# Performance work log

Hardware: AMD Instinct MI355X
Metric: run time of the kernel (lower is better)

Reference implementation:

```python
import jax, jax.numpy as jnp
import numpy as np

OT_REG = 0.1
OT_ITERS = 10
LN_EPS = 1e-5


def layernorm(x, g, b):
    m = jnp.mean(x, axis=-1, keepdims=True)
    v = jnp.mean((x - m) ** 2, axis=-1, keepdims=True)
    return (x - m) * jax.lax.rsqrt(v + LN_EPS) * g + b


def sinkhorn(C, epsilon, iters):
    # standard Sinkhorn: kernel exp(C/eps), alternate row/col normalization
    Q = jnp.exp(C / epsilon)  # [Na,B,La,Lb]
    def body(_, Q):
        Q = Q / jnp.sum(Q, axis=-1, keepdims=True)
        Q = Q / jnp.sum(Q, axis=-2, keepdims=True)
        return Q
    return jax.lax.fori_loop(0, iters, body, Q)


def setup_inputs() -> dict:
    key = jax.random.key(0)
    ks = jax.random.split(key, 16)
    Na, La, B, Lb, Din, H = 32, 32, 64, 32, 768, 768
    s = 0.02
    return {
        "entity_cls": jax.random.normal(ks[0], (Na, Din), jnp.float32),
        "entity_tokens": jax.random.normal(ks[1], (Na, La, Din), jnp.float32),
        "mention_cls": jax.random.normal(ks[2], (B, Din), jnp.float32),
        "mention_tokens": jax.random.normal(ks[3], (B, Lb, Din), jnp.float32),
        "Wq": jax.random.normal(ks[4], (Din, H), jnp.float32) * s,
        "bq": jnp.zeros((H,), jnp.float32),
        "Wk": jax.random.normal(ks[5], (Din, H), jnp.float32) * s,
        "bk": jnp.zeros((H,), jnp.float32),
        "Wv": jax.random.normal(ks[6], (Din, H), jnp.float32) * s,
        "bv": jnp.zeros((H,), jnp.float32),
        "ln1_g": jnp.ones((H,), jnp.float32),
        "ln1_b": jnp.zeros((H,), jnp.float32),
        "Wcls": jax.random.normal(ks[7], (Din, H), jnp.float32) * s,
        "bcls": jnp.zeros((H,), jnp.float32),
        "Wsp": jax.random.normal(ks[8], (H, 1), jnp.float32) * s,
        "bsp": jnp.zeros((1,), jnp.float32),
        "ln2_g": jnp.ones((H,), jnp.float32),
        "ln2_b": jnp.zeros((H,), jnp.float32),
    }


def reference(entity_cls, entity_tokens, mention_cls, mention_tokens,
              Wq, bq, Wk, bk, Wv, bv, ln1_g, ln1_b,
              Wcls, bcls, Wsp, bsp, ln2_g, ln2_b):
    # projections
    q = entity_tokens @ Wq + bq      # [Na,La,H]
    k = mention_tokens @ Wk + bk     # [B,Lb,H]
    v = mention_tokens @ Wv + bv     # [B,Lb,H]

    # cross-batch cosine similarity: [Na,B,La,Lb]
    qn = q / jnp.maximum(jnp.linalg.norm(q, axis=-1, keepdims=True), 1e-8)
    kn = k / jnp.maximum(jnp.linalg.norm(k, axis=-1, keepdims=True), 1e-8)
    C = jnp.einsum('aid,bjd->abij', qn, kn)

    # Sinkhorn on detached cost (torch uses C.detach())
    T = sinkhorn(jax.lax.stop_gradient(C), OT_REG, OT_ITERS)
    # F.normalize(dim=-1): L2 normalize last dim
    T = T / jnp.maximum(jnp.linalg.norm(T, axis=-1, keepdims=True), 1e-12)

    # attention + residual + layernorm: [Na,B,La,H]
    attended = jnp.einsum('abij,bjd->abid', T, v) + q[:, None, :, :]
    attended = layernorm(attended, ln1_g, ln1_b)

    # softpool over token dim (-2)
    w = jax.nn.softmax(attended @ Wsp + bsp, axis=-2)   # [Na,B,La,1]
    pooled = jnp.sum(attended * w, axis=-2)             # [Na,B,H]
    context = layernorm(pooled, ln2_g, ln2_b)

    # matching scores
    ecls = entity_cls @ Wcls + bcls                     # [Na,H]
    g2l = jnp.sum(ecls[:, None, :] * context, axis=-1)  # [Na,B]
    g2l = g2l.T                                         # [B,Na]
    g2g = mention_cls @ entity_cls.T                    # [B,Na]
    return (g2l + g2g) * 0.5
```

## Files before the change

### kernel.cpp

```cpp
#include <hip/hip_runtime.h>
#include <math.h>


typedef __attribute__((ext_vector_type(8))) short bfrag8;
typedef __attribute__((ext_vector_type(4))) float f32x4;

__device__ __forceinline__ unsigned short f2bf(float x) {
  union { float f; unsigned u; } v; v.f = x;
  unsigned r = v.u + 0x7fffu + ((v.u >> 16) & 1u);
  return (unsigned short)(r >> 16);
}

__global__ __launch_bounds__(256) void prep_kernel(
    const float* __restrict__ a0, const float* __restrict__ a1, const float* __restrict__ a2,
    unsigned short* __restrict__ o0, unsigned short* __restrict__ o1, unsigned short* __restrict__ o2,
    float* __restrict__ nrm,
    const float* __restrict__ W0, const float* __restrict__ W1,
    const float* __restrict__ W2, const float* __restrict__ W3,
    unsigned short* __restrict__ T0, unsigned short* __restrict__ T1,
    unsigned short* __restrict__ T2, unsigned short* __restrict__ T3) {
  __shared__ float t[32][33];
  int bx = blockIdx.x;
  if (bx < 2331) {
    if (bx < 2328) {
      const float* in; unsigned short* out; int i, n4;
      if (bx < 768)       { in = a0; out = o0; i = bx * 256 + threadIdx.x;          n4 = 196608; }
      else if (bx < 2304) { in = a1; out = o1; i = (bx - 768) * 256 + threadIdx.x;  n4 = 393216; }
      else                { in = a2; out = o2; i = (bx - 2304) * 256 + threadIdx.x; n4 = 6144; }
      if (i >= n4) return;
      float4 f = ((const float4*)in)[i];
      ushort4 o;
      o.x = f2bf(f.x); o.y = f2bf(f.y); o.z = f2bf(f.z); o.w = f2bf(f.w);
      ((ushort4*)out)[i] = o;
    } else {
      int i = (bx - 2328) * 256 + threadIdx.x;
      if (i < 768) ((float4*)nrm)[i] = make_float4(0.f, 0.f, 0.f, 0.f);
    }
    return;
  }
  int idx = bx - 2331;
  int z = idx / 576, r2 = idx % 576;
  int tby = r2 / 24, tbx = r2 % 24;
  const float* W = (z == 0) ? W0 : (z == 1) ? W1 : (z == 2) ? W2 : W3;
  unsigned short* O = (z == 0) ? T0 : (z == 1) ? T1 : (z == 2) ? T2 : T3;
  const int gx = tbx * 32, gy = tby * 32;
  const int tx = threadIdx.x & 31, ty = threadIdx.x >> 5;
#pragma unroll
  for (int u = 0; u < 4; ++u) {
    int row = ty + u * 8;
    t[row][tx] = W[(size_t)(gy + row) * 768 + gx + tx];
  }
  __syncthreads();
#pragma unroll
  for (int u = 0; u < 4; ++u) {
    int row = ty + u * 8;
    O[(size_t)(gx + row) * 768 + gy + tx] = f2bf(t[tx][row]);
  }
}

__global__ __launch_bounds__(256) void proj_gemm_kernel(
    const unsigned short* __restrict__ Ae, const unsigned short* __restrict__ Am,
    const unsigned short* __restrict__ Acls,
    const unsigned short* __restrict__ WqT, const unsigned short* __restrict__ WkT,
    const unsigned short* __restrict__ WvT, const unsigned short* __restrict__ WclsT,
    const float* __restrict__ bq, const float* __restrict__ bk,
    const float* __restrict__ bv, const float* __restrict__ bcls,
    unsigned short* __restrict__ qb, unsigned short* __restrict__ qT,
    unsigned short* __restrict__ kb, unsigned short* __restrict__ vT,
    float* __restrict__ ecls, float* __restrict__ iq_sq, float* __restrict__ ik_sq) {
  const int z = blockIdx.z;
  const int M = (z == 0) ? 1024 : (z == 3) ? 32 : 2048;
  const int bm = blockIdx.y * 128;
  if (bm >= M) return;
  const unsigned short* A = (z == 3) ? Acls : (z == 0) ? Ae : Am;
  const unsigned short* B = (z == 0) ? WqT : (z == 1) ? WkT : (z == 2) ? WvT : WclsT;
  const float* bias = (z == 0) ? bq : (z == 1) ? bk : (z == 2) ? bv : bcls;

  __shared__ unsigned short As[128 * 64];
  __shared__ unsigned short Bs[128 * 64];
  const int t = threadIdx.x;
  const int bn = blockIdx.x * 128;
  const int l = t & 63, w = t >> 6;
  const int wm = w & 1, wn = w >> 1;

  f32x4 acc[4][4];
#pragma unroll
  for (int mi = 0; mi < 4; ++mi)
#pragma unroll
    for (int nj = 0; nj < 4; ++nj) { f32x4 zz = {0.f, 0.f, 0.f, 0.f}; acc[mi][nj] = zz; }

  for (int k0 = 0; k0 < 768; k0 += 64) {
    __syncthreads();
#pragma unroll
    for (int u = 0; u < 4; ++u) {
      int c = t + u * 256;
      int row = c >> 3, kc = c & 7;
      int gm = bm + row; gm = gm < M ? gm : M - 1;
      int4 av = *(const int4*)(A + (size_t)gm * 768 + k0 + kc * 8);
      *(int4*)(As + row * 64 + ((kc ^ (row & 7)) * 8)) = av;
      int4 bv4 = *(const int4*)(B + (size_t)(bn + row) * 768 + k0 + kc * 8);
      *(int4*)(Bs + row * 64 + ((kc ^ (row & 7)) * 8)) = bv4;
    }
    __syncthreads();
#pragma unroll
    for (int kk = 0; kk < 2; ++kk) {
      bfrag8 af[4], bf[4];
      const int kc = kk * 4 + (l >> 4);
#pragma unroll
      for (int mi = 0; mi < 4; ++mi) {
        int arow = wm * 64 + mi * 16 + (l & 15);
        af[mi] = *(const bfrag8*)(As + arow * 64 + ((kc ^ (arow & 7)) * 8));
      }
#pragma unroll
      for (int nj = 0; nj < 4; ++nj) {
        int brow = wn * 64 + nj * 16 + (l & 15);
        bf[nj] = *(const bfrag8*)(Bs + brow * 64 + ((kc ^ (brow & 7)) * 8));
      }
#pragma unroll
      for (int mi = 0; mi < 4; ++mi)
#pragma unroll
        for (int nj = 0; nj < 4; ++nj)
          acc[mi][nj] = __builtin_amdgcn_mfma_f32_16x16x32_bf16(af[mi], bf[nj], acc[mi][nj], 0, 0, 0);
    }
  }

  const int col = l & 15, rq = l >> 4;
  float p[4][4] = {};
#pragma unroll
  for (int mi = 0; mi < 4; ++mi) {
#pragma unroll
    for (int nj = 0; nj < 4; ++nj) {
      int gn = bn + wn * 64 + nj * 16 + col;
      float bs = bias[gn];
#pragma unroll
      for (int r = 0; r < 4; ++r) {
        int gm = bm + wm * 64 + mi * 16 + rq * 4 + r;
        if (gm >= M) continue;
        float val = acc[mi][nj][r] + bs;
        if (z < 2) p[mi][r] += val * val;
        unsigned short bfv = f2bf(val);
        if (z == 0) {
          qb[(size_t)gm * 768 + gn] = bfv;
          int at = gm >> 5, j = gm & 31;
          qT[((size_t)at * 768 + gn) * 32 + j] = bfv;
        } else if (z == 1) kb[(size_t)gm * 768 + gn] = bfv;
        else if (z == 2) {
          int bb = gm >> 5, j = gm & 31;
          vT[((size_t)bb * 768 + gn) * 32 + j] = bfv;
        } else ecls[(size_t)gm * 768 + gn] = val;
      }
    }
  }
  if (z < 2) {
    float* nrm = (z == 0) ? iq_sq : ik_sq;
#pragma unroll
    for (int mi = 0; mi < 4; ++mi)
#pragma unroll
      for (int r = 0; r < 4; ++r) {
        float s = p[mi][r];
        s += __shfl_xor(s, 1); s += __shfl_xor(s, 2);
        s += __shfl_xor(s, 4); s += __shfl_xor(s, 8);
        if (col == 0) {
          int gm = bm + wm * 64 + mi * 16 + rq * 4 + r;
          atomicAdd(&nrm[gm], s);
        }
      }
  }
}

__global__ __launch_bounds__(256) void cos_sink_kernel(
    const unsigned short* __restrict__ qb, const unsigned short* __restrict__ kb,
    const float* __restrict__ iq_sq, const float* __restrict__ ik_sq,
    unsigned short* __restrict__ Tg,
    const float* __restrict__ ln1_g, const float* __restrict__ ln1_b,
    const float* __restrict__ Wsp, const float* __restrict__ bsp,
    const float* __restrict__ ln2_g, const float* __restrict__ ln2_b,
    const float* __restrict__ ecls,
    const float* __restrict__ entity_cls, const float* __restrict__ mention_cls,
    float4* __restrict__ aux4, float4* __restrict__ cons, float* __restrict__ g2g) {
  __shared__ unsigned short As[128 * 64];
  __shared__ unsigned short Bs[64 * 64];
  __shared__ float ldsIq[128], ldsIk[64];
  const int t = threadIdx.x;

  if (blockIdx.y == 8) {
    float* redf = (float*)As;
    const int a2 = blockIdx.x;
    float sgw = 0.f, sbw = 0.f, sga = 0.f, sba = 0.f;
#pragma unroll
    for (int cc = 0; cc < 3; ++cc) {
      int h = t + cc * 256;
      float g1 = ln1_g[h], b1 = ln1_b[h], wsp = Wsp[h];
      float ec = ecls[(size_t)a2 * 768 + h];
      float gw = g1 * wsp;
      float gab = ln2_g[h] * ec;
      float4 v4; v4.x = gw; v4.y = g1; v4.z = b1; v4.w = gab;
      aux4[(size_t)a2 * 768 + h] = v4;
      sgw += gw; sbw += b1 * wsp; sga += gab; sba += ln2_b[h] * ec;
    }
#pragma unroll
    for (int m = 1; m < 64; m <<= 1) {
      sgw += __shfl_xor(sgw, m); sbw += __shfl_xor(sbw, m);
      sga += __shfl_xor(sga, m); sba += __shfl_xor(sba, m);
    }
    const int wv = t >> 6, ln = t & 63;
    if (ln == 0) { redf[wv * 4] = sgw; redf[wv * 4 + 1] = sbw; redf[wv * 4 + 2] = sga; redf[wv * 4 + 3] = sba; }
    __syncthreads();
    if (t == 0) {
      float4 c;
      c.x = redf[0] + redf[4] + redf[8] + redf[12];
      c.y = redf[1] + redf[5] + redf[9] + redf[13] + bsp[0];
      c.z = redf[2] + redf[6] + redf[10] + redf[14];
      c.w = redf[3] + redf[7] + redf[11] + redf[15];
      cons[a2] = c;
    }
    const float* ea = entity_cls + (size_t)a2 * 768;
    for (int bb = wv; bb < 64; bb += 4) {
      const float* mbp = mention_cls + (size_t)bb * 768;
      float s = 0.f;
#pragma unroll
      for (int u = 0; u < 12; ++u) s += mbp[ln * 12 + u] * ea[ln * 12 + u];
#pragma unroll
      for (int m = 1; m < 64; m <<= 1) s += __shfl_xor(s, m);
      if (ln == 0) g2g[bb * 32 + a2] = s;
    }
    return;
  }

  const int bn = blockIdx.x * 64, bm = blockIdx.y * 128;
  const int l = t & 63, w = t >> 6;
  const int wm = w & 1, wn = w >> 1;
  const int cg = l & 15, rq = l >> 4;

  if (t < 128) ldsIq[t] = iq_sq[bm + t];
  else if (t < 192) ldsIk[t - 128] = ik_sq[bn + t - 128];

  f32x4 acc[4][2];
#pragma unroll
  for (int mi = 0; mi < 4; ++mi)
#pragma unroll
    for (int nj = 0; nj < 2; ++nj) { f32x4 zz = {0.f, 0.f, 0.f, 0.f}; acc[mi][nj] = zz; }

  for (int k0 = 0; k0 < 768; k0 += 64) {
    __syncthreads();
#pragma unroll
    for (int u = 0; u < 4; ++u) {
      int c = t + u * 256;
      int row = c >> 3, kc = c & 7;
      int4 av = *(const int4*)(qb + (size_t)(bm + row) * 768 + k0 + kc * 8);
      *(int4*)(As + row * 64 + ((kc ^ (row & 7)) * 8)) = av;
    }
#pragma unroll
    for (int u = 0; u < 2; ++u) {
      int c = t + u * 256;
      int row = c >> 3, kc = c & 7;
      int4 bv4 = *(const int4*)(kb + (size_t)(bn + row) * 768 + k0 + kc * 8);
      *(int4*)(Bs + row * 64 + ((kc ^ (row & 7)) * 8)) = bv4;
    }
    __syncthreads();
#pragma unroll
    for (int kk = 0; kk < 2; ++kk) {
      bfrag8 af[4], bf[2];
      const int kc = kk * 4 + rq;
#pragma unroll
      for (int mi = 0; mi < 4; ++mi) {
        int arow = wm * 64 + mi * 16 + cg;
        af[mi] = *(const bfrag8*)(As + arow * 64 + ((kc ^ (arow & 7)) * 8));
      }
#pragma unroll
      for (int nj = 0; nj < 2; ++nj) {
        int brow = wn * 32 + nj * 16 + cg;
        bf[nj] = *(const bfrag8*)(Bs + brow * 64 + ((kc ^ (brow & 7)) * 8));
      }
#pragma unroll
      for (int mi = 0; mi < 4; ++mi)
#pragma unroll
        for (int nj = 0; nj < 2; ++nj)
          acc[mi][nj] = __builtin_amdgcn_mfma_f32_16x16x32_bf16(af[mi], bf[nj], acc[mi][nj], 0, 0, 0);
    }
  }

  float irow[4][4], icol[2];
#pragma unroll
  for (int mi = 0; mi < 4; ++mi)
#pragma unroll
    for (int r = 0; r < 4; ++r) {
      float s = ldsIq[wm * 64 + mi * 16 + rq * 4 + r];
      irow[mi][r] = 1.0f / fmaxf(sqrtf(s), 1e-8f);
    }
#pragma unroll
  for (int nj = 0; nj < 2; ++nj) {
    float s = ldsIk[wn * 32 + nj * 16 + cg];
    icol[nj] = 1.0f / fmaxf(sqrtf(s), 1e-8f);
  }
#pragma unroll
  for (int mi = 0; mi < 4; ++mi)
#pragma unroll
    for (int nj = 0; nj < 2; ++nj)
#pragma unroll
      for (int r = 0; r < 4; ++r)
        acc[mi][nj][r] = __expf(acc[mi][nj][r] * irow[mi][r] * icol[nj] * 10.0f);

  for (int it = 0; it < 10; ++it) {
#pragma unroll
    for (int mi = 0; mi < 4; ++mi)
#pragma unroll
      for (int r = 0; r < 4; ++r) {
        float rs = acc[mi][0][r] + acc[mi][1][r];
        rs += __shfl_xor(rs, 1); rs += __shfl_xor(rs, 2);
        rs += __shfl_xor(rs, 4); rs += __shfl_xor(rs, 8);
        float rinv = __builtin_amdgcn_rcpf(rs);
        acc[mi][0][r] *= rinv; acc[mi][1][r] *= rinv;
      }
#pragma unroll
    for (int ta = 0; ta < 2; ++ta)
#pragma unroll
      for (int nj = 0; nj < 2; ++nj) {
        float cs = acc[2 * ta][nj][0] + acc[2 * ta][nj][1] + acc[2 * ta][nj][2] + acc[2 * ta][nj][3]
                 + acc[2 * ta + 1][nj][0] + acc[2 * ta + 1][nj][1] + acc[2 * ta + 1][nj][2] + acc[2 * ta + 1][nj][3];
        cs += __shfl_xor(cs, 16); cs += __shfl_xor(cs, 32);
        float cinv = __builtin_amdgcn_rcpf(cs);
#pragma unroll
        for (int mi2 = 0; mi2 < 2; ++mi2)
#pragma unroll
          for (int r = 0; r < 4; ++r) acc[2 * ta + mi2][nj][r] *= cinv;
      }
  }

#pragma unroll
  for (int mi = 0; mi < 4; ++mi)
#pragma unroll
    for (int r = 0; r < 4; ++r) {
      float ss = acc[mi][0][r] * acc[mi][0][r] + acc[mi][1][r] * acc[mi][1][r];
      ss += __shfl_xor(ss, 1); ss += __shfl_xor(ss, 2);
      ss += __shfl_xor(ss, 4); ss += __shfl_xor(ss, 8);
      float tinv = 1.0f / fmaxf(sqrtf(ss), 1e-12f);
      acc[mi][0][r] *= tinv; acc[mi][1][r] *= tinv;
    }

  const int b_idx = (bn >> 5) + wn;
#pragma unroll
  for (int mi = 0; mi < 4; ++mi) {
    const int a_idx = (bm >> 5) + wm * 2 + (mi >> 1);
    unsigned short* base = Tg + (((size_t)b_idx * 32 + a_idx) << 10);
    const int ri0 = (mi & 1) * 16 + rq * 4;
#pragma unroll
    for (int nj = 0; nj < 2; ++nj)
#pragma unroll
      for (int r = 0; r < 4; ++r)
        base[(ri0 + r) * 32 + nj * 16 + cg] = f2bf(acc[mi][nj][r]);
  }
}

__global__ __launch_bounds__(256) void attn_kernel(
    const unsigned short* __restrict__ Tg,
    const unsigned short* __restrict__ vT,
    const unsigned short* __restrict__ qT,
    const float4* __restrict__ aux4,
    const float4* __restrict__ cons,
    const float* __restrict__ g2g,
    float* __restrict__ out) {
  const int t = threadIdx.x;
  const int w = t >> 6, l = t & 63;
  const int pair = blockIdx.x * 4 + w;
  const int b = pair >> 5, a = pair & 31;
  const int cg = l & 15, rq = l >> 4;

  const unsigned short* Tp = Tg + ((size_t)pair << 10);
  bfrag8 af[2], afI[2];
#pragma unroll
  for (int mi = 0; mi < 2; ++mi) {
    int row = mi * 16 + cg;
    af[mi] = *(const bfrag8*)(Tp + row * 32 + rq * 8);
    bfrag8 fI;
#pragma unroll
    for (int u = 0; u < 8; ++u) fI[u] = (row == rq * 8 + u) ? (short)0x3F80 : (short)0;
    afI[mi] = fI;
  }

  const unsigned short* vTb = vT + (size_t)b * 768 * 32;
  const unsigned short* qTa = qT + (size_t)a * 768 * 32;
  const float4* auxa = aux4 + (size_t)a * 768;
  const float4 cc4 = cons[a];

  float s1[2][4] = {}, s2[2][4] = {}, a1[2][4] = {};
#pragma unroll 4
  for (int nj = 0; nj < 48; ++nj) {
    int h = nj * 16 + cg;
    bfrag8 vf = *(const bfrag8*)(vTb + (size_t)h * 32 + rq * 8);
    bfrag8 qf = *(const bfrag8*)(qTa + (size_t)h * 32 + rq * 8);
    float gw = auxa[h].x;
#pragma unroll
    for (int mi = 0; mi < 2; ++mi) {
      f32x4 zz = {0.f, 0.f, 0.f, 0.f};
      f32x4 p = __builtin_amdgcn_mfma_f32_16x16x32_bf16(af[mi], vf, zz, 0, 0, 0);
      f32x4 x4 = __builtin_amdgcn_mfma_f32_16x16x32_bf16(afI[mi], qf, p, 0, 0, 0);
#pragma unroll
      for (int r = 0; r < 4; ++r) {
        float x = x4[r];
        s1[mi][r] += x; s2[mi][r] += x * x; a1[mi][r] += x * gw;
      }
    }
  }
#pragma unroll
  for (int m = 1; m < 16; m <<= 1) {
#pragma unroll
    for (int mi = 0; mi < 2; ++mi)
#pragma unroll
      for (int r = 0; r < 4; ++r) {
        s1[mi][r] += __shfl_xor(s1[mi][r], m);
        s2[mi][r] += __shfl_xor(s2[mi][r], m);
        a1[mi][r] += __shfl_xor(a1[mi][r], m);
      }
  }

  float uu[2][4], c0 = 0.f;
  {
    float mean[2][4], rstd[2][4], logit[2][4];
#pragma unroll
    for (int mi = 0; mi < 2; ++mi)
#pragma unroll
      for (int r = 0; r < 4; ++r) {
        float m1 = s1[mi][r] * (1.0f / 768.0f);
        float var = s2[mi][r] * (1.0f / 768.0f) - m1 * m1;
        float rs = rsqrtf(var + 1e-5f);
        mean[mi][r] = m1; rstd[mi][r] = rs;
        logit[mi][r] = rs * (a1[mi][r] - m1 * cc4.x) + cc4.y;
      }
    float mx = logit[0][0];
#pragma unroll
    for (int mi = 0; mi < 2; ++mi)
#pragma unroll
      for (int r = 0; r < 4; ++r) mx = fmaxf(mx, logit[mi][r]);
    mx = fmaxf(mx, __shfl_xor(mx, 16)); mx = fmaxf(mx, __shfl_xor(mx, 32));
    float se = 0.f, ee[2][4];
#pragma unroll
    for (int mi = 0; mi < 2; ++mi)
#pragma unroll
      for (int r = 0; r < 4; ++r) { ee[mi][r] = __expf(logit[mi][r] - mx); se += ee[mi][r]; }
    se += __shfl_xor(se, 16); se += __shfl_xor(se, 32);
    const float sinv = __builtin_amdgcn_rcpf(se);
#pragma unroll
    for (int mi = 0; mi < 2; ++mi)
#pragma unroll
      for (int r = 0; r < 4; ++r) {
        uu[mi][r] = ee[mi][r] * sinv * rstd[mi][r];
        c0 += uu[mi][r] * mean[mi][r];
      }
    c0 += __shfl_xor(c0, 16); c0 += __shfl_xor(c0, 32);
  }

  float ps = 0.f, pq = 0.f, spc = 0.f;
#pragma unroll 4
  for (int nj = 0; nj < 48; ++nj) {
    int h = nj * 16 + cg;
    bfrag8 vf = *(const bfrag8*)(vTb + (size_t)h * 32 + rq * 8);
    bfrag8 qf = *(const bfrag8*)(qTa + (size_t)h * 32 + rq * 8);
    float4 av = auxa[h];
    float pp = 0.f;
#pragma unroll
    for (int mi = 0; mi < 2; ++mi) {
      f32x4 zz = {0.f, 0.f, 0.f, 0.f};
      f32x4 p = __builtin_amdgcn_mfma_f32_16x16x32_bf16(af[mi], vf, zz, 0, 0, 0);
      f32x4 x4 = __builtin_amdgcn_mfma_f32_16x16x32_bf16(afI[mi], qf, p, 0, 0, 0);
#pragma unroll
      for (int r = 0; r < 4; ++r) pp += uu[mi][r] * x4[r];
    }
    pp += __shfl_xor(pp, 16); pp += __shfl_xor(pp, 32);
    float pooled = av.y * (pp - c0) + av.z;
    ps += pooled; pq += pooled * pooled; spc += pooled * av.w;
  }
#pragma unroll
  for (int m = 1; m < 16; m <<= 1) {
    ps += __shfl_xor(ps, m); pq += __shfl_xor(pq, m); spc += __shfl_xor(spc, m);
  }
  const float m2 = ps * (1.0f / 768.0f);
  const float var2 = pq * (1.0f / 768.0f) - m2 * m2;
  const float rs2 = rsqrtf(var2 + 1e-5f);
  float tot = rs2 * (spc - m2 * cc4.z) + cc4.w + g2g[b * 32 + a];
  if (l == 0) out[b * 32 + a] = 0.5f * tot;
}

extern "C" void kernel_launch(void* const* d_in, const int* in_sizes, int n_in,
                              void* d_out, int out_size, void* d_ws, size_t ws_size,
                              hipStream_t stream) {
  const float* entity_cls     = (const float*)d_in[0];
  const float* entity_tokens  = (const float*)d_in[1];
  const float* mention_cls    = (const float*)d_in[2];
  const float* mention_tokens = (const float*)d_in[3];
  const float* Wq = (const float*)d_in[4];   const float* bq = (const float*)d_in[5];
  const float* Wk = (const float*)d_in[6];   const float* bk = (const float*)d_in[7];
  const float* Wv = (const float*)d_in[8];   const float* bv = (const float*)d_in[9];
  const float* ln1_g = (const float*)d_in[10]; const float* ln1_b = (const float*)d_in[11];
  const float* Wcls = (const float*)d_in[12];  const float* bcls = (const float*)d_in[13];
  const float* Wsp = (const float*)d_in[14];   const float* bsp = (const float*)d_in[15];
  const float* ln2_g = (const float*)d_in[16]; const float* ln2_b = (const float*)d_in[17];
  float* out = (float*)d_out;

  float* ws    = (float*)d_ws;
  float* ecls  = ws;
  float* iq_sq = ecls + 24576;
  float* ik_sq = iq_sq + 1024;
  float4* aux4 = (float4*)(ik_sq + 2048);
  float4* cons = aux4 + 24576;
  float* g2g   = (float*)(cons + 32);
  unsigned short* qb = (unsigned short*)(g2g + 2048);
  unsigned short* qT = qb + 786432;
  unsigned short* kb = qT + 786432;
  unsigned short* vT = kb + 1572864;
  char* R = (char*)(vT + 1572864);
  unsigned short* Ae    = (unsigned short*)R;
  unsigned short* Am    = Ae + 786432;
  unsigned short* Acls  = Am + 1572864;
  unsigned short* WqT   = Acls + 24576;
  unsigned short* WkT   = WqT + 589824;
  unsigned short* WvT   = WkT + 589824;
  unsigned short* WclsT = WvT + 589824;
  unsigned short* Tg = (unsigned short*)R;

  dim3 blk(256);
  prep_kernel<<<dim3(4635), blk, 0, stream>>>(
      entity_tokens, mention_tokens, entity_cls, Ae, Am, Acls, iq_sq,
      Wq, Wk, Wv, Wcls, WqT, WkT, WvT, WclsT);
  proj_gemm_kernel<<<dim3(6, 16, 4), blk, 0, stream>>>(
      Ae, Am, Acls, WqT, WkT, WvT, WclsT, bq, bk, bv, bcls,
      qb, qT, kb, vT, ecls, iq_sq, ik_sq);
  cos_sink_kernel<<<dim3(32, 9), blk, 0, stream>>>(
      qb, kb, iq_sq, ik_sq, Tg,
      ln1_g, ln1_b, Wsp, bsp, ln2_g, ln2_b, ecls, entity_cls, mention_cls,
      aux4, cons, g2g);
  attn_kernel<<<dim3(512), blk, 0, stream>>>(
      Tg, vT, qT, aux4, cons, g2g, out);
}
```

Measured before the change: 197.8 us.

## Stage mention V tile in LDS and split aux array into compact per-field buffers

The attention kernel now maps each block to one mention b and four entities, copying that mention's 48KB transposed V slab into shared memory once and reading V fragments from LDS in both passes. The float4 aux array is replaced by a shared gw vector, direct ln1 gamma/beta loads, and a per-entity gab array, which cuts redundant global traffic. The cost is 48KB of LDS per block, which may limit occupancy, plus a block-wide sync before compute.

```diff
diff --git a/kernel.cpp b/kernel.cpp
--- a/kernel.cpp
+++ b/kernel.cpp
@@ -177,7 +177,8 @@
     const float* __restrict__ ln2_g, const float* __restrict__ ln2_b,
     const float* __restrict__ ecls,
     const float* __restrict__ entity_cls, const float* __restrict__ mention_cls,
-    float4* __restrict__ aux4, float4* __restrict__ cons, float* __restrict__ g2g) {
+    float* __restrict__ gwv, float* __restrict__ auxgab,
+    float4* __restrict__ cons, float* __restrict__ g2g) {
   __shared__ unsigned short As[128 * 64];
   __shared__ unsigned short Bs[64 * 64];
   __shared__ float ldsIq[128], ldsIk[64];
@@ -194,8 +195,8 @@
       float ec = ecls[(size_t)a2 * 768 + h];
       float gw = g1 * wsp;
       float gab = ln2_g[h] * ec;
-      float4 v4; v4.x = gw; v4.y = g1; v4.z = b1; v4.w = gab;
-      aux4[(size_t)a2 * 768 + h] = v4;
+      if (a2 == 0) gwv[h] = gw;
+      auxgab[(size_t)a2 * 768 + h] = gab;
       sgw += gw; sbw += b1 * wsp; sga += gab; sba += ln2_b[h] * ec;
     }
 #pragma unroll
@@ -356,15 +357,27 @@
     const unsigned short* __restrict__ Tg,
     const unsigned short* __restrict__ vT,
     const unsigned short* __restrict__ qT,
-    const float4* __restrict__ aux4,
+    const float* __restrict__ gwv,
+    const float* __restrict__ ln1_g, const float* __restrict__ ln1_b,
+    const float* __restrict__ auxgab,
     const float4* __restrict__ cons,
     const float* __restrict__ g2g,
     float* __restrict__ out) {
+  __shared__ unsigned short vLds[768 * 32];
   const int t = threadIdx.x;
   const int w = t >> 6, l = t & 63;
-  const int pair = blockIdx.x * 4 + w;
-  const int b = pair >> 5, a = pair & 31;
+  const int b = blockIdx.x >> 3;
+  const int a = ((blockIdx.x & 7) << 2) + w;
+  const int pair = b * 32 + a;
   const int cg = l & 15, rq = l >> 4;
+
+  {
+    const int4* src = (const int4*)(vT + (size_t)b * 768 * 32);
+    int4* dst = (int4*)vLds;
+#pragma unroll
+    for (int u = 0; u < 12; ++u) dst[t + u * 256] = src[t + u * 256];
+  }
+  __syncthreads();
 
   const unsigned short* Tp = Tg + ((size_t)pair << 10);
   bfrag8 af[2], afI[2];
@@ -378,18 +391,16 @@
     afI[mi] = fI;
   }
 
-  const unsigned short* vTb = vT + (size_t)b * 768 * 32;
   const unsigned short* qTa = qT + (size_t)a * 768 * 32;
-  const float4* auxa = aux4 + (size_t)a * 768;
   const float4 cc4 = cons[a];
 
   float s1[2][4] = {}, s2[2][4] = {}, a1[2][4] = {};
 #pragma unroll 4
   for (int nj = 0; nj < 48; ++nj) {
     int h = nj * 16 + cg;
-    bfrag8 vf = *(const bfrag8*)(vTb + (size_t)h * 32 + rq * 8);
+    bfrag8 vf = *(const bfrag8*)(vLds + h * 32 + rq * 8);
     bfrag8 qf = *(const bfrag8*)(qTa + (size_t)h * 32 + rq * 8);
-    float gw = auxa[h].x;
+    float gw = gwv[h];
 #pragma unroll
     for (int mi = 0; mi < 2; ++mi) {
       f32x4 zz = {0.f, 0.f, 0.f, 0.f};
@@ -450,13 +461,13 @@
     c0 += __shfl_xor(c0, 16); c0 += __shfl_xor(c0, 32);
   }
 
+  const float* gabp = auxgab + (size_t)a * 768;
   float ps = 0.f, pq = 0.f, spc = 0.f;
 #pragma unroll 4
   for (int nj = 0; nj < 48; ++nj) {
     int h = nj * 16 + cg;
-    bfrag8 vf = *(const bfrag8*)(vTb + (size_t)h * 32 + rq * 8);
+    bfrag8 vf = *(const bfrag8*)(vLds + h * 32 + rq * 8);
     bfrag8 qf = *(const bfrag8*)(qTa + (size_t)h * 32 + rq * 8);
-    float4 av = auxa[h];
     float pp = 0.f;
 #pragma unroll
     for (int mi = 0; mi < 2; ++mi) {
@@ -467,8 +478,8 @@
       for (int r = 0; r < 4; ++r) pp += uu[mi][r] * x4[r];
     }
     pp += __shfl_xor(pp, 16); pp += __shfl_xor(pp, 32);
-    float pooled = av.y * (pp - c0) + av.z;
-    ps += pooled; pq += pooled * pooled; spc += pooled * av.w;
+    float pooled = ln1_g[h] * (pp - c0) + ln1_b[h];
+    ps += pooled; pq += pooled * pooled; spc += pooled * gabp[h];
   }
 #pragma unroll
   for (int m = 1; m < 16; m <<= 1) {
@@ -497,14 +508,15 @@
   const float* ln2_g = (const float*)d_in[16]; const float* ln2_b = (const float*)d_in[17];
   float* out = (float*)d_out;
 
-  float* ws    = (float*)d_ws;
-  float* ecls  = ws;
-  float* iq_sq = ecls + 24576;
-  float* ik_sq = iq_sq + 1024;
-  float4* aux4 = (float4*)(ik_sq + 2048);
-  float4* cons = aux4 + 24576;
-  float* g2g   = (float*)(cons + 32);
-  unsigned short* qb = (unsigned short*)(g2g + 2048);
+  float* ws     = (float*)d_ws;
+  float* ecls   = ws;
+  float* iq_sq  = ecls + 24576;
+  float* ik_sq  = iq_sq + 1024;
+  float* gwv    = ik_sq + 2048;
+  float* auxgab = gwv + 768;
+  float* g2g    = auxgab + 24576;
+  float4* cons  = (float4*)(g2g + 2048);
+  unsigned short* qb = (unsigned short*)(cons + 32);
   unsigned short* qT = qb + 786432;
   unsigned short* kb = qT + 786432;
   unsigned short* vT = kb + 1572864;
@@ -528,7 +540,7 @@
   cos_sink_kernel<<<dim3(32, 9), blk, 0, stream>>>(
       qb, kb, iq_sq, ik_sq, Tg,
       ln1_g, ln1_b, Wsp, bsp, ln2_g, ln2_b, ecls, entity_cls, mention_cls,
-      aux4, cons, g2g);
+      gwv, auxgab, cons, g2g);
   attn_kernel<<<dim3(512), blk, 0, stream>>>(
-      Tg, vT, qT, aux4, cons, g2g, out);
+      Tg, vT, qT, gwv, ln1_g, ln1_b, auxgab, cons, g2g, out);
 }
```

Result: faster. 185.8 us (-6.1%).
